# Performance work log

Measured on AMD Instinct MI355X. Metric: run time of the kernel, lower is better.

The kernel has to match this reference:

```python
import jax, jax.numpy as jnp
import numpy as np

E = 1024
H = 16
HD = 64
LN_EPS = 1e-5


def _layernorm(x, g, b):
    mu = jnp.mean(x, axis=-1, keepdims=True)
    var = jnp.mean((x - mu) ** 2, axis=-1, keepdims=True)
    return (x - mu) * jax.lax.rsqrt(var + LN_EPS) * g + b


def _positional(L):
    # PositionalEncoding: stepper = 1/10000^(arange(0,E,2)/E); cat(sin, cos) -> [L, E]
    stepper = 1.0 / (10000.0 ** (jnp.arange(0, E, 2, dtype=jnp.float32) / E))
    args = jnp.arange(L, dtype=jnp.float32)[:, None] * stepper[None, :]  # [L, E/2]
    return jnp.concatenate([jnp.sin(args), jnp.cos(args)], axis=1)  # [L, E]


def setup_inputs() -> dict:
    key = jax.random.key(0)
    ks = jax.random.split(key, 8)
    s = 1.0 / np.sqrt(E)
    return {
        "sequences": jax.random.normal(ks[0], (4, 2048, E), dtype=jnp.float32),
        "W_q": jax.random.normal(ks[1], (E, E), dtype=jnp.float32) * s,
        "W_k": jax.random.normal(ks[2], (E, E), dtype=jnp.float32) * s,
        "W_v": jax.random.normal(ks[3], (E, E), dtype=jnp.float32) * s,
        "W_o": jax.random.normal(ks[4], (E, E), dtype=jnp.float32) * s,
        "ln1_g": jnp.ones((E,), jnp.float32),
        "ln1_b": jnp.zeros((E,), jnp.float32),
        "lin_W": jax.random.normal(ks[5], (E, E), dtype=jnp.float32) * s,  # torch Linear weight [out,in]
        "lin_b": jnp.zeros((E,), jnp.float32),
        "ln2_g": jnp.ones((E,), jnp.float32),
        "ln2_b": jnp.zeros((E,), jnp.float32),
    }


def reference(sequences, W_q, W_k, W_v, W_o, ln1_g, ln1_b, lin_W, lin_b, ln2_g, ln2_b):
    B, L, _ = sequences.shape
    x = sequences + _positional(L)[None]  # add positional embeddings
    # projections (no bias)
    q = (x @ W_q).reshape(B, L, H, HD).transpose(0, 2, 1, 3)  # [B,H,L,hd]
    k = (x @ W_k).reshape(B, L, H, HD).transpose(0, 2, 1, 3)
    v = (x @ W_v).reshape(B, L, H, HD).transpose(0, 2, 1, 3)
    # linear (softmax-free) attention: (Q K^T / sqrt(hd)) V
    scores = jnp.einsum("bhqd,bhkd->bhqk", q, k) / jnp.sqrt(jnp.float32(HD))
    ctx = jnp.einsum("bhqk,bhkd->bhqd", scores, v)
    ctx = ctx.transpose(0, 2, 1, 3).reshape(B, L, E)
    attn_out = ctx @ W_o
    h = _layernorm(x + attn_out, ln1_g, ln1_b)
    ff = jax.nn.relu(h @ lin_W.T + lin_b)
    return _layernorm(ff + h, ln2_g, ln2_b)
```

## Files before the change

kernel.cpp:

```cpp
#include <hip/hip_runtime.h>
#include <cstdint>

typedef unsigned short u16;
typedef __bf16 bf16x8 __attribute__((ext_vector_type(8)));
typedef float f32x4 __attribute__((ext_vector_type(4)));

__device__ __forceinline__ u16 f2bf(float f) {
    unsigned u = __float_as_uint(f);
    u += 0x7fffu + ((u >> 16) & 1u);
    return (u16)(u >> 16);
}
__device__ __forceinline__ float bf2f(u16 h) {
    return __uint_as_float(((unsigned)h) << 16);
}

__device__ __forceinline__ void lds16(const void* g, void* l) {
    __builtin_amdgcn_global_load_lds(
        (const __attribute__((address_space(1))) void*)g,
        (__attribute__((address_space(3))) void*)l, 16, 0, 0);
}

__device__ __forceinline__ float pos_term(int l, int e) {
    const float c = -13.287712379549449f / 512.0f;
    int ii = e & 511;
    float st  = exp2f(c * (float)ii);
    float arg = (float)l * st;
    return (e < 512) ? sinf(arg) : cosf(arg);
}

__global__ __launch_bounds__(256) void prep_x(const float* __restrict__ seq,
                                              u16* __restrict__ xb) {
    size_t i = (size_t)blockIdx.x * 256 + threadIdx.x;
    int e4 = (int)(i & 255) * 4;
    int l  = (int)((i >> 8) & 2047);
    float4 s = ((const float4*)seq)[i];
    float v[4] = {s.x, s.y, s.z, s.w};
#pragma unroll
    for (int j = 0; j < 4; j++) v[j] += pos_term(l, e4 + j);
    ushort4 ob; ob.x = f2bf(v[0]); ob.y = f2bf(v[1]); ob.z = f2bf(v[2]); ob.w = f2bf(v[3]);
    ((ushort4*)xb)[i] = ob;
}

__global__ void prep_w(const float* __restrict__ wq, const float* __restrict__ wk,
                       const float* __restrict__ wv, const float* __restrict__ wl,
                       u16* __restrict__ wt) {
    int mat = blockIdx.z;
    const float* src = (mat == 0) ? wq : (mat == 1) ? wk : (mat == 2) ? wv : wl;
    u16* dst = wt + (size_t)mat * 1024 * 1024;
    int tx = threadIdx.x, ty = threadIdx.y;
    if (mat == 0 || mat == 3) {
        int col = blockIdx.x * 32 + tx, row0 = blockIdx.y * 32;
#pragma unroll
        for (int j = 0; j < 32; j += 8)
            dst[(size_t)(row0 + ty + j) * 1024 + col] = f2bf(src[(size_t)(row0 + ty + j) * 1024 + col]);
    } else {
        __shared__ float tile[32][33];
        int col = blockIdx.x * 32 + tx, row0 = blockIdx.y * 32;
#pragma unroll
        for (int j = 0; j < 32; j += 8)
            tile[ty + j][tx] = src[(size_t)(row0 + ty + j) * 1024 + col];
        __syncthreads();
        int col2 = blockIdx.y * 32 + tx, row20 = blockIdx.x * 32;
#pragma unroll
        for (int j = 0; j < 32; j += 8)
            dst[(size_t)(row20 + ty + j) * 1024 + col2] = f2bf(tile[tx][ty + j]);
    }
}

template <int EPI>
__global__ __launch_bounds__(512) void gemm8p(const u16* __restrict__ A,
                                              const u16* __restrict__ Bt,
                                              void* __restrict__ Cv,
                                              const float* __restrict__ bias,
                                              int N, int K, int lda, size_t bstride) {
    __shared__ __align__(16) u16 lds[49152];
    const int t = threadIdx.x;
    const int ntn = N >> 8;
    const int nwg = gridDim.x;
    int bid = (int)blockIdx.x;
    bid = (bid & 7) * (nwg >> 3) + (bid >> 3);
    const int tm = bid / ntn, tn = bid - tm * ntn;
    const size_t m0 = (size_t)tm << 7, n0 = (size_t)tn << 8;
    const int w = t >> 6, lane = t & 63;
    const int wr = w >> 2, wc = w & 3;
    const u16* Bt_e = Bt + (bstride ? (m0 >> 11) * bstride : 0);

    const int r0 = t >> 3;
    const int ksrc = (t & 7) ^ (r0 & 7);
    const u16* sA0 = A + (m0 + r0) * (size_t)lda + ksrc * 8;
    const u16* sA1 = sA0 + (size_t)64 * lda;
    const u16* sB0 = Bt_e + (n0 + r0) * (size_t)K + ksrc * 8;
    const u16* sB1 = sB0 + (size_t)64 * K;
    const u16* sB2 = sB0 + (size_t)128 * K;
    const u16* sB3 = sB0 + (size_t)192 * K;
    u16* dstW = lds + (w << 9);

    const int ao = ((wr << 6) | (lane & 15)) << 6;
    const int bo = 8192 + ((((wc << 6) | (lane & 15))) << 6);
    const int kx = lane & 7;
    const int ks0 = (((lane >> 4) ^ kx) << 3);
    const int ks1 = (((4 + (lane >> 4)) ^ kx) << 3);

    f32x4 acc[4][4];
#pragma unroll
    for (int i = 0; i < 4; i++)
#pragma unroll
        for (int j = 0; j < 4; j++)
#pragma unroll
            for (int r = 0; r < 4; r++) acc[i][j][r] = 0.0f;

    const int NT = K >> 6;
    lds16(sA0, dstW);          lds16(sA1, dstW + 4096);
    lds16(sB0, dstW + 8192);   lds16(sB1, dstW + 12288);
    lds16(sB2, dstW + 16384);  lds16(sB3, dstW + 20480);

    for (int kt = 0; kt < NT; kt++) {
        const int b = kt & 1;
        asm volatile("" ::: "memory");
        if (kt + 1 < NT) {
            const size_t ko = (size_t)(kt + 1) << 6;
            u16* d = dstW + (b ^ 1) * 24576;
            lds16(sA0 + ko, d);          lds16(sA1 + ko, d + 4096);
            lds16(sB0 + ko, d + 8192);   lds16(sB1 + ko, d + 12288);
            lds16(sB2 + ko, d + 16384);  lds16(sB3 + ko, d + 20480);
            asm volatile("s_waitcnt vmcnt(6)" ::: "memory");
        } else {
            asm volatile("s_waitcnt vmcnt(0)" ::: "memory");
        }
        __builtin_amdgcn_s_barrier();
        asm volatile("" ::: "memory");
        const u16* Lb = lds + b * 24576;
#pragma unroll
        for (int kc = 0; kc < 2; kc++) {
            const int ksl = kc ? ks1 : ks0;
            bf16x8 af[4], bfr[4];
#pragma unroll
            for (int i = 0; i < 4; i++)
                af[i] = *reinterpret_cast<const bf16x8*>(Lb + ao + i * 1024 + ksl);
#pragma unroll
            for (int j = 0; j < 4; j++)
                bfr[j] = *reinterpret_cast<const bf16x8*>(Lb + bo + j * 1024 + ksl);
            __builtin_amdgcn_s_setprio(1);
#pragma unroll
            for (int i = 0; i < 4; i++)
#pragma unroll
                for (int j = 0; j < 4; j++)
                    acc[i][j] = __builtin_amdgcn_mfma_f32_16x16x32_bf16(af[i], bfr[j], acc[i][j], 0, 0, 0);
            __builtin_amdgcn_s_setprio(0);
        }
        asm volatile("" ::: "memory");
        __builtin_amdgcn_s_barrier();
    }

    const int crow = (lane >> 4) << 2, ccol = lane & 15;
#pragma unroll
    for (int i = 0; i < 4; i++)
#pragma unroll
        for (int j = 0; j < 4; j++) {
            size_t row = m0 + (wr << 6) + (i << 4) + crow;
            size_t col = n0 + (wc << 6) + (j << 4) + ccol;
#pragma unroll
            for (int r = 0; r < 4; r++) {
                float v = acc[i][j][r];
                if (EPI == 3) { v += bias[col]; v = fmaxf(v, 0.0f); }
                if (EPI == 0) ((float*)Cv)[(row + r) * (size_t)N + col] = v;
                else          ((u16*)Cv)[(row + r) * (size_t)N + col] = f2bf(v);
            }
        }
}

__global__ __launch_bounds__(256) void ktv_kernel(const u16* __restrict__ kv,
                                                  float* __restrict__ part) {
    const int bh = blockIdx.x, split = blockIdx.y;
    const int b = bh >> 4, h = bh & 15;
    const u16* Kp = kv + (size_t)b * 2048 * 2048 + h * 64;
    const u16* Vp = Kp + 1024;
    __shared__ float ks[8][64], vs[8][64];
    float acc[16];
#pragma unroll
    for (int i = 0; i < 16; i++) acc[i] = 0.0f;
    const int t = threadIdx.x, r = t >> 4, c = t & 15;
    const int lr = t >> 5, lc = (t & 31) * 2;
    for (int l0 = split * 128; l0 < split * 128 + 128; l0 += 8) {
        unsigned kk = *(const unsigned*)(Kp + (size_t)(l0 + lr) * 2048 + lc);
        unsigned vv = *(const unsigned*)(Vp + (size_t)(l0 + lr) * 2048 + lc);
        ks[lr][lc] = bf2f((u16)kk); ks[lr][lc + 1] = bf2f((u16)(kk >> 16));
        vs[lr][lc] = bf2f((u16)vv); vs[lr][lc + 1] = bf2f((u16)(vv >> 16));
        __syncthreads();
#pragma unroll
        for (int i = 0; i < 8; i++) {
            float kvr[4], vw[4];
#pragma unroll
            for (int a = 0; a < 4; a++) { kvr[a] = ks[i][r + 16 * a]; vw[a] = vs[i][c + 16 * a]; }
#pragma unroll
            for (int a = 0; a < 4; a++)
#pragma unroll
                for (int q = 0; q < 4; q++) acc[a * 4 + q] += kvr[a] * vw[q];
        }
        __syncthreads();
    }
    float* o = part + ((size_t)split * 64 + bh) * 4096;
#pragma unroll
    for (int a = 0; a < 4; a++)
#pragma unroll
        for (int q = 0; q < 4; q++) o[(r + 16 * a) * 64 + (c + 16 * q)] = acc[a * 4 + q];
}

__global__ __launch_bounds__(256) void ktv_reduce(const float* __restrict__ part,
                                                  float* __restrict__ ktv) {
    int i = blockIdx.x * 256 + threadIdx.x;
    float s = 0.0f;
#pragma unroll
    for (int sp = 0; sp < 16; sp++) s += part[(size_t)sp * 262144 + i];
    ktv[i] = s;
}

__global__ __launch_bounds__(256) void wprime_kernel(const float* __restrict__ ktv,
                                                     const float* __restrict__ Wo,
                                                     u16* __restrict__ wp) {
    const int n = blockIdx.x * 256 + threadIdx.x;
    const int h = blockIdx.y, b = blockIdx.z;
    const float* kt = ktv + ((size_t)(b * 16 + h) << 12);
    float acc[64];
#pragma unroll
    for (int i = 0; i < 64; i++) acc[i] = 0.0f;
    for (int j = 0; j < 64; j++) {
        float w = Wo[(size_t)(h * 64 + j) * 1024 + n];
#pragma unroll
        for (int i = 0; i < 64; i++) acc[i] += kt[i * 64 + j] * w;
    }
    u16* o = wp + ((size_t)b << 20) + (size_t)n * 1024 + h * 64;
    u16 ob[64];
#pragma unroll
    for (int i = 0; i < 64; i++) ob[i] = f2bf(acc[i] * 0.125f);
#pragma unroll
    for (int i = 0; i < 8; i++)
        ((uint4*)o)[i] = ((const uint4*)ob)[i];
}

__global__ __launch_bounds__(256) void ln_pos(const float* __restrict__ seq,
                                              const u16* __restrict__ attn,
                                              const float* __restrict__ g,
                                              const float* __restrict__ be,
                                              float* __restrict__ outF,
                                              u16* __restrict__ outB) {
    __shared__ float sm[4];
    const int row = blockIdx.x, t = threadIdx.x;
    const int l = row & 2047, e4 = t * 4;
    const float4 a = ((const float4*)(seq + (size_t)row * 1024))[t];
    const ushort4 ab = ((const ushort4*)(attn + (size_t)row * 1024))[t];
    float x0 = a.x + pos_term(l, e4 + 0) + bf2f(ab.x);
    float x1 = a.y + pos_term(l, e4 + 1) + bf2f(ab.y);
    float x2 = a.z + pos_term(l, e4 + 2) + bf2f(ab.z);
    float x3 = a.w + pos_term(l, e4 + 3) + bf2f(ab.w);
    float s = x0 + x1 + x2 + x3;
#pragma unroll
    for (int off = 32; off > 0; off >>= 1) s += __shfl_down(s, off);
    if ((t & 63) == 0) sm[t >> 6] = s;
    __syncthreads();
    const float mean = (sm[0] + sm[1] + sm[2] + sm[3]) * (1.0f / 1024.0f);
    __syncthreads();
    x0 -= mean; x1 -= mean; x2 -= mean; x3 -= mean;
    float s2 = x0 * x0 + x1 * x1 + x2 * x2 + x3 * x3;
#pragma unroll
    for (int off = 32; off > 0; off >>= 1) s2 += __shfl_down(s2, off);
    if ((t & 63) == 0) sm[t >> 6] = s2;
    __syncthreads();
    const float var = (sm[0] + sm[1] + sm[2] + sm[3]) * (1.0f / 1024.0f);
    const float rs = rsqrtf(var + 1e-5f);
    const float4 gv = ((const float4*)g)[t];
    const float4 bv = ((const float4*)be)[t];
    float y0 = x0 * rs * gv.x + bv.x;
    float y1 = x1 * rs * gv.y + bv.y;
    float y2 = x2 * rs * gv.z + bv.z;
    float y3 = x3 * rs * gv.w + bv.w;
    float4 o; o.x = y0; o.y = y1; o.z = y2; o.w = y3;
    ((float4*)(outF + (size_t)row * 1024))[t] = o;
    ushort4 ob; ob.x = f2bf(y0); ob.y = f2bf(y1); ob.z = f2bf(y2); ob.w = f2bf(y3);
    ((ushort4*)(outB + (size_t)row * 1024))[t] = ob;
}

__global__ __launch_bounds__(256) void ln2_kernel(const u16* __restrict__ ff,
                                                  const float* __restrict__ h1,
                                                  const float* __restrict__ g,
                                                  const float* __restrict__ be,
                                                  float* __restrict__ outF) {
    __shared__ float sm[4];
    const int row = blockIdx.x, t = threadIdx.x;
    const ushort4 fb = ((const ushort4*)(ff + (size_t)row * 1024))[t];
    const float4 b = ((const float4*)(h1 + (size_t)row * 1024))[t];
    float x0 = bf2f(fb.x) + b.x, x1 = bf2f(fb.y) + b.y;
    float x2 = bf2f(fb.z) + b.z, x3 = bf2f(fb.w) + b.w;
    float s = x0 + x1 + x2 + x3;
#pragma unroll
    for (int off = 32; off > 0; off >>= 1) s += __shfl_down(s, off);
    if ((t & 63) == 0) sm[t >> 6] = s;
    __syncthreads();
    const float mean = (sm[0] + sm[1] + sm[2] + sm[3]) * (1.0f / 1024.0f);
    __syncthreads();
    x0 -= mean; x1 -= mean; x2 -= mean; x3 -= mean;
    float s2 = x0 * x0 + x1 * x1 + x2 * x2 + x3 * x3;
#pragma unroll
    for (int off = 32; off > 0; off >>= 1) s2 += __shfl_down(s2, off);
    if ((t & 63) == 0) sm[t >> 6] = s2;
    __syncthreads();
    const float var = (sm[0] + sm[1] + sm[2] + sm[3]) * (1.0f / 1024.0f);
    const float rs = rsqrtf(var + 1e-5f);
    const float4 gv = ((const float4*)g)[t];
    const float4 bv = ((const float4*)be)[t];
    float4 o;
    o.x = x0 * rs * gv.x + bv.x;
    o.y = x1 * rs * gv.y + bv.y;
    o.z = x2 * rs * gv.z + bv.z;
    o.w = x3 * rs * gv.w + bv.w;
    ((float4*)(outF + (size_t)row * 1024))[t] = o;
}

extern "C" void kernel_launch(void* const* d_in, const int* in_sizes, int n_in,
                              void* d_out, int out_size, void* d_ws, size_t ws_size,
                              hipStream_t stream) {
    const float* seq = (const float*)d_in[0];
    const float* Wq  = (const float*)d_in[1];
    const float* Wk  = (const float*)d_in[2];
    const float* Wv  = (const float*)d_in[3];
    const float* Wo  = (const float*)d_in[4];
    const float* g1  = (const float*)d_in[5];
    const float* b1  = (const float*)d_in[6];
    const float* Wl  = (const float*)d_in[7];
    const float* bl  = (const float*)d_in[8];
    const float* g2  = (const float*)d_in[9];
    const float* b2  = (const float*)d_in[10];

    char* ws = (char*)d_ws;
    const size_t MB = 1024 * 1024;
    u16*   x_bf  = (u16*)(ws + 0);
    u16*   wt    = (u16*)(ws + 16 * MB);
    u16*   kv    = (u16*)(ws + 24 * MB);
    float* h1f   = (float*)(ws + 24 * MB);
    float* kpart = (float*)(ws + 56 * MB);
    u16*   attn  = (u16*)(ws + 56 * MB);
    float* ktv   = (float*)(ws + 72 * MB);
    u16*   wpr   = (u16*)(ws + 73 * MB);
    u16*   wcomb = (u16*)(ws + 81 * MB);
    u16*   h1b   = (u16*)(ws + 89 * MB);
    u16*   ffb   = (u16*)(ws + 105 * MB);

    prep_x<<<dim3(8192), dim3(256), 0, stream>>>(seq, x_bf);
    prep_w<<<dim3(32, 32, 4), dim3(32, 8), 0, stream>>>(Wq, Wk, Wv, Wl, wt);
    gemm8p<2><<<dim3(512), dim3(512), 0, stream>>>(x_bf, wt + (size_t)1 * MB, kv, nullptr,
                                                   2048, 1024, 1024, 0);
    ktv_kernel<<<dim3(64, 16), dim3(256), 0, stream>>>(kv, kpart);
    ktv_reduce<<<dim3(1024), dim3(256), 0, stream>>>(kpart, ktv);
    wprime_kernel<<<dim3(4, 16, 4), dim3(256), 0, stream>>>(ktv, Wo, wpr);
    gemm8p<2><<<dim3(128), dim3(512), 0, stream>>>(wpr, wt, wcomb, nullptr,
                                                   1024, 1024, 1024, 0);
    gemm8p<2><<<dim3(256), dim3(512), 0, stream>>>(x_bf, wcomb, attn, nullptr,
                                                   1024, 1024, 1024, (size_t)1024 * 1024);
    ln_pos<<<dim3(8192), dim3(256), 0, stream>>>(seq, attn, g1, b1, h1f, h1b);
    gemm8p<3><<<dim3(256), dim3(512), 0, stream>>>(h1b, wt + (size_t)3 * MB, ffb,
                                                   bl, 1024, 1024, 1024, 0);
    ln2_kernel<<<dim3(8192), dim3(256), 0, stream>>>(ffb, h1f, g2, b2, (float*)d_out);
}
```

Baseline: 212.6 us.

## Add 256x256 GEMM for K/V projection and drop fp32 LN intermediates

Adds a new gemm256 kernel with 256x256 output tiles, double-buffered LDS staging and four-phase MFMA scheduling, and uses it for the K/V projection in place of the 128x256 gemm8p. This raises data reuse per block and halves the block count. LayerNorm 1 now reads the bf16 x instead of recomputing the fp32 sequence plus positional term, and it writes only a bf16 output. LayerNorm 2 reads that bf16 residual, which removes the fp32 h1 buffer traffic but lowers the precision of the residual path.

```diff
diff --git a/kernel.cpp b/kernel.cpp
--- a/kernel.cpp
+++ b/kernel.cpp
@@ -65,6 +65,121 @@
         for (int j = 0; j < 32; j += 8)
             dst[(size_t)(row20 + ty + j) * 1024 + col2] = f2bf(tile[tx][ty + j]);
     }
+}
+
+__global__ __launch_bounds__(512) void gemm256(const u16* __restrict__ A,
+                                               const u16* __restrict__ Bt,
+                                               u16* __restrict__ C,
+                                               int N, int K, int lda) {
+    __shared__ __align__(16) u16 lds[65536];
+    const int t = threadIdx.x;
+    const int ntn = N >> 8;
+    const int nwg = gridDim.x;
+    int bid = (int)blockIdx.x;
+    bid = (bid & 7) * (nwg >> 3) + (bid >> 3);
+    const int tm = bid / ntn, tn = bid - tm * ntn;
+    const size_t m0 = (size_t)tm << 8, n0 = (size_t)tn << 8;
+    const int w = t >> 6, lane = t & 63;
+    const int wr = w >> 2, wc = w & 3;
+
+    const int r0 = t >> 3;
+    const int ksrc = (t & 7) ^ (r0 & 7);
+    const u16* sA0 = A + (m0 + r0) * (size_t)lda + ksrc * 8;
+    const u16* sA1 = sA0 + (size_t)128 * lda;
+    const u16* sB0 = Bt + (n0 + r0) * (size_t)K + ksrc * 8;
+    const u16* sB1 = sB0 + (size_t)128 * K;
+    const size_t stA = (size_t)64 * lda, stB = (size_t)64 * K;
+
+#define STAGE(bb, hh, src, str, ko)                                           \
+    do {                                                                      \
+        u16* d_ = lds + (bb) * 32768 + (hh) * 8192 + (w << 9);                \
+        lds16((src) + (ko), d_);                                              \
+        lds16((src) + (ko) + (str), d_ + 4096);                               \
+    } while (0)
+
+    const int kx = lane & 7;
+    const int ks0 = (((lane >> 4) ^ kx) << 3);
+    const int ks1 = (((4 + (lane >> 4)) ^ kx) << 3);
+    const int arow = (wr << 7) + (lane & 15);
+    const int brow = (wc << 6) + (lane & 15);
+
+    f32x4 acc[8][4];
+#pragma unroll
+    for (int i = 0; i < 8; i++)
+#pragma unroll
+        for (int j = 0; j < 4; j++)
+#pragma unroll
+            for (int r = 0; r < 4; r++) acc[i][j][r] = 0.0f;
+
+    const int NT = K >> 6;
+    STAGE(0, 0, sA0, stA, 0); STAGE(0, 1, sA1, stA, 0);
+    STAGE(0, 2, sB0, stB, 0); STAGE(0, 3, sB1, stB, 0);
+
+    for (int kt = 0; kt < NT; kt++) {
+        const int b = kt & 1;
+        const u16* Lb = lds + b * 32768;
+        const size_t ko = (size_t)(kt + 1) << 6;
+        const bool pf = (kt + 1 < NT);
+        bf16x8 af[4][2], bfr[2][2];
+#pragma unroll
+        for (int ph = 0; ph < 4; ph++) {
+            const int mq = ph >> 1, nq = ph & 1;
+            if (ph == 0) {
+                if (pf) {
+                    STAGE(b ^ 1, 0, sA0, stA, ko);
+                    STAGE(b ^ 1, 1, sA1, stA, ko);
+                    asm volatile("s_waitcnt vmcnt(4)" ::: "memory");
+                } else {
+                    asm volatile("s_waitcnt vmcnt(0)" ::: "memory");
+                }
+                __builtin_amdgcn_s_barrier();
+                asm volatile("" ::: "memory");
+            }
+            if (ph == 0 || ph == 2) {
+#pragma unroll
+                for (int i = 0; i < 4; i++) {
+                    const int ar = (arow + mq * 64 + i * 16) << 6;
+                    af[i][0] = *reinterpret_cast<const bf16x8*>(Lb + ar + ks0);
+                    af[i][1] = *reinterpret_cast<const bf16x8*>(Lb + ar + ks1);
+                }
+            }
+#pragma unroll
+            for (int j = 0; j < 2; j++) {
+                const int br = 16384 + ((brow + nq * 32 + j * 16) << 6);
+                bfr[j][0] = *reinterpret_cast<const bf16x8*>(Lb + br + ks0);
+                bfr[j][1] = *reinterpret_cast<const bf16x8*>(Lb + br + ks1);
+            }
+            if (ph == 1 && pf) STAGE(b ^ 1, 2, sB0, stB, ko);
+            if (ph == 2 && pf) STAGE(b ^ 1, 3, sB1, stB, ko);
+            asm volatile("" ::: "memory");
+            if (ph != 0) __builtin_amdgcn_s_barrier();
+            __builtin_amdgcn_s_setprio(1);
+#pragma unroll
+            for (int kc = 0; kc < 2; kc++)
+#pragma unroll
+                for (int i = 0; i < 4; i++)
+#pragma unroll
+                    for (int j = 0; j < 2; j++)
+                        acc[mq * 4 + i][nq * 2 + j] = __builtin_amdgcn_mfma_f32_16x16x32_bf16(
+                            af[i][kc], bfr[j][kc], acc[mq * 4 + i][nq * 2 + j], 0, 0, 0);
+            __builtin_amdgcn_s_setprio(0);
+            asm volatile("" ::: "memory");
+            __builtin_amdgcn_s_barrier();
+        }
+    }
+#undef STAGE
+
+    const int crow = (lane >> 4) << 2, ccol = lane & 15;
+#pragma unroll
+    for (int i = 0; i < 8; i++)
+#pragma unroll
+        for (int j = 0; j < 4; j++) {
+            size_t row = m0 + (wr << 7) + (i << 4) + crow;
+            size_t col = n0 + (wc << 6) + (j << 4) + ccol;
+#pragma unroll
+            for (int r = 0; r < 4; r++)
+                C[(row + r) * (size_t)N + col] = f2bf(acc[i][j][r]);
+        }
 }
 
 template <int EPI>
@@ -163,8 +278,7 @@
             for (int r = 0; r < 4; r++) {
                 float v = acc[i][j][r];
                 if (EPI == 3) { v += bias[col]; v = fmaxf(v, 0.0f); }
-                if (EPI == 0) ((float*)Cv)[(row + r) * (size_t)N + col] = v;
-                else          ((u16*)Cv)[(row + r) * (size_t)N + col] = f2bf(v);
+                ((u16*)Cv)[(row + r) * (size_t)N + col] = f2bf(v);
             }
         }
 }
@@ -238,21 +352,17 @@
         ((uint4*)o)[i] = ((const uint4*)ob)[i];
 }
 
-__global__ __launch_bounds__(256) void ln_pos(const float* __restrict__ seq,
-                                              const u16* __restrict__ attn,
-                                              const float* __restrict__ g,
-                                              const float* __restrict__ be,
-                                              float* __restrict__ outF,
-                                              u16* __restrict__ outB) {
+__global__ __launch_bounds__(256) void ln1_kernel(const u16* __restrict__ xb,
+                                                  const u16* __restrict__ attn,
+                                                  const float* __restrict__ g,
+                                                  const float* __restrict__ be,
+                                                  u16* __restrict__ outB) {
     __shared__ float sm[4];
     const int row = blockIdx.x, t = threadIdx.x;
-    const int l = row & 2047, e4 = t * 4;
-    const float4 a = ((const float4*)(seq + (size_t)row * 1024))[t];
-    const ushort4 ab = ((const ushort4*)(attn + (size_t)row * 1024))[t];
-    float x0 = a.x + pos_term(l, e4 + 0) + bf2f(ab.x);
-    float x1 = a.y + pos_term(l, e4 + 1) + bf2f(ab.y);
-    float x2 = a.z + pos_term(l, e4 + 2) + bf2f(ab.z);
-    float x3 = a.w + pos_term(l, e4 + 3) + bf2f(ab.w);
+    const ushort4 xv = ((const ushort4*)(xb + (size_t)row * 1024))[t];
+    const ushort4 av = ((const ushort4*)(attn + (size_t)row * 1024))[t];
+    float x0 = bf2f(xv.x) + bf2f(av.x), x1 = bf2f(xv.y) + bf2f(av.y);
+    float x2 = bf2f(xv.z) + bf2f(av.z), x3 = bf2f(xv.w) + bf2f(av.w);
     float s = x0 + x1 + x2 + x3;
 #pragma unroll
     for (int off = 32; off > 0; off >>= 1) s += __shfl_down(s, off);
@@ -270,27 +380,25 @@
     const float rs = rsqrtf(var + 1e-5f);
     const float4 gv = ((const float4*)g)[t];
     const float4 bv = ((const float4*)be)[t];
-    float y0 = x0 * rs * gv.x + bv.x;
-    float y1 = x1 * rs * gv.y + bv.y;
-    float y2 = x2 * rs * gv.z + bv.z;
-    float y3 = x3 * rs * gv.w + bv.w;
-    float4 o; o.x = y0; o.y = y1; o.z = y2; o.w = y3;
-    ((float4*)(outF + (size_t)row * 1024))[t] = o;
-    ushort4 ob; ob.x = f2bf(y0); ob.y = f2bf(y1); ob.z = f2bf(y2); ob.w = f2bf(y3);
+    ushort4 ob;
+    ob.x = f2bf(x0 * rs * gv.x + bv.x);
+    ob.y = f2bf(x1 * rs * gv.y + bv.y);
+    ob.z = f2bf(x2 * rs * gv.z + bv.z);
+    ob.w = f2bf(x3 * rs * gv.w + bv.w);
     ((ushort4*)(outB + (size_t)row * 1024))[t] = ob;
 }
 
 __global__ __launch_bounds__(256) void ln2_kernel(const u16* __restrict__ ff,
-                                                  const float* __restrict__ h1,
+                                                  const u16* __restrict__ h1,
                                                   const float* __restrict__ g,
                                                   const float* __restrict__ be,
                                                   float* __restrict__ outF) {
     __shared__ float sm[4];
     const int row = blockIdx.x, t = threadIdx.x;
-    const ushort4 fb = ((const ushort4*)(ff + (size_t)row * 1024))[t];
-    const float4 b = ((const float4*)(h1 + (size_t)row * 1024))[t];
-    float x0 = bf2f(fb.x) + b.x, x1 = bf2f(fb.y) + b.y;
-    float x2 = bf2f(fb.z) + b.z, x3 = bf2f(fb.w) + b.w;
+    const ushort4 fv = ((const ushort4*)(ff + (size_t)row * 1024))[t];
+    const ushort4 hv = ((const ushort4*)(h1 + (size_t)row * 1024))[t];
+    float x0 = bf2f(fv.x) + bf2f(hv.x), x1 = bf2f(fv.y) + bf2f(hv.y);
+    float x2 = bf2f(fv.z) + bf2f(hv.z), x3 = bf2f(fv.w) + bf2f(hv.w);
     float s = x0 + x1 + x2 + x3;
 #pragma unroll
     for (int off = 32; off > 0; off >>= 1) s += __shfl_down(s, off);
@@ -336,7 +444,6 @@
     u16*   x_bf  = (u16*)(ws + 0);
     u16*   wt    = (u16*)(ws + 16 * MB);
     u16*   kv    = (u16*)(ws + 24 * MB);
-    float* h1f   = (float*)(ws + 24 * MB);
     float* kpart = (float*)(ws + 56 * MB);
     u16*   attn  = (u16*)(ws + 56 * MB);
     float* ktv   = (float*)(ws + 72 * MB);
@@ -347,8 +454,8 @@
 
     prep_x<<<dim3(8192), dim3(256), 0, stream>>>(seq, x_bf);
     prep_w<<<dim3(32, 32, 4), dim3(32, 8), 0, stream>>>(Wq, Wk, Wv, Wl, wt);
-    gemm8p<2><<<dim3(512), dim3(512), 0, stream>>>(x_bf, wt + (size_t)1 * MB, kv, nullptr,
-                                                   2048, 1024, 1024, 0);
+    gemm256<<<dim3(256), dim3(512), 0, stream>>>(x_bf, wt + (size_t)1 * MB, kv,
+                                                 2048, 1024, 1024);
     ktv_kernel<<<dim3(64, 16), dim3(256), 0, stream>>>(kv, kpart);
     ktv_reduce<<<dim3(1024), dim3(256), 0, stream>>>(kpart, ktv);
     wprime_kernel<<<dim3(4, 16, 4), dim3(256), 0, stream>>>(ktv, Wo, wpr);
@@ -356,8 +463,8 @@
                                                    1024, 1024, 1024, 0);
     gemm8p<2><<<dim3(256), dim3(512), 0, stream>>>(x_bf, wcomb, attn, nullptr,
                                                    1024, 1024, 1024, (size_t)1024 * 1024);
-    ln_pos<<<dim3(8192), dim3(256), 0, stream>>>(seq, attn, g1, b1, h1f, h1b);
+    ln1_kernel<<<dim3(8192), dim3(256), 0, stream>>>(x_bf, attn, g1, b1, h1b);
     gemm8p<3><<<dim3(256), dim3(512), 0, stream>>>(h1b, wt + (size_t)3 * MB, ffb,
                                                    bl, 1024, 1024, 1024, 0);
-    ln2_kernel<<<dim3(8192), dim3(256), 0, stream>>>(ffb, h1f, g2, b2, (float*)d_out);
-}
+    ln2_kernel<<<dim3(8192), dim3(256), 0, stream>>>(ffb, h1b, g2, b2, (float*)d_out);
+}
```

New measurement: 201.8 us. -5.1%, faster.
